# Performance work log

Measured on AMD Instinct MI355X. Metric: run time of the kernel, lower is better.

## Reference

```python
import math
import jax, jax.numpy as jnp
import numpy as np

N_HEAD = 16


def setup_inputs() -> dict:
    key = jax.random.key(0)
    ks = jax.random.split(key, 6)
    B, T, C = 4, 2048, 1024
    hs = C // N_HEAD
    block_size = 2048
    x = jax.random.normal(ks[0], (B, T, C), dtype=jnp.float32)
    c_attn_w = jax.random.normal(ks[1], (C, 3 * C), dtype=jnp.float32) * 0.02
    c_attn_b = jnp.zeros((3 * C,), dtype=jnp.float32)
    c_proj_w = jax.random.normal(ks[2], (C, C), dtype=jnp.float32) * (0.02 * (2 * 24) ** -0.5)
    c_proj_b = jnp.zeros((C,), dtype=jnp.float32)
    wpe = jax.random.normal(ks[3], (block_size, hs), dtype=jnp.float32) * 0.02
    return {"x": x, "c_attn_w": c_attn_w, "c_attn_b": c_attn_b,
            "c_proj_w": c_proj_w, "c_proj_b": c_proj_b, "wpe": wpe}


def reference(x, c_attn_w, c_attn_b, c_proj_w, c_proj_b, wpe):
    B, T, C = x.shape
    hs = C // N_HEAD
    # fused QKV projection
    qkv = x @ c_attn_w + c_attn_b            # [B, T, 3C]
    q, k, v = jnp.split(qkv, 3, axis=-1)
    pos_emb = wpe[:T]                        # [T, hs]
    # NOTE: faithful to original — raw reshape (not transpose) before the add
    q = (q.reshape(B, N_HEAD, T, hs) + pos_emb).reshape(B, T, N_HEAD, hs)
    k = (k.reshape(B, N_HEAD, T, hs) + pos_emb).reshape(B, T, N_HEAD, hs)
    v = v.reshape(B, T, N_HEAD, hs)
    # vanilla causal attention
    qt = jnp.transpose(q, (0, 2, 1, 3))      # [B, H, T, hs]
    kt = jnp.transpose(k, (0, 2, 3, 1))      # [B, H, hs, T]
    vt = jnp.transpose(v, (0, 2, 1, 3))      # [B, H, T, hs]
    att = qt @ kt / math.sqrt(hs)            # [B, H, T, T]
    causal = jnp.tril(jnp.ones((T, T), dtype=bool))
    att = jnp.where(causal, att, float('-inf'))
    att = jax.nn.softmax(att, axis=-1)
    y = att @ vt                             # [B, H, T, hs]
    y = jnp.transpose(y, (0, 2, 1, 3)).reshape(B, T, C)
    return y @ c_proj_w + c_proj_b
```

## Files before the change

kernel.cpp:

```cpp
#include <hip/hip_runtime.h>

typedef __attribute__((ext_vector_type(8))) short s16x8;
typedef __attribute__((ext_vector_type(4))) float f32x4;
typedef __attribute__((ext_vector_type(4))) unsigned short u16x4;

#define AS1 __attribute__((address_space(1)))
#define AS3 __attribute__((address_space(3)))

__device__ __forceinline__ unsigned short f2bf(float f) {
    union { float f; unsigned u; } c; c.f = f;
    return (unsigned short)((c.u + 0x7FFFu + ((c.u >> 16) & 1u)) >> 16);
}

__global__ void k_f32_to_bf16(const float* __restrict__ src,
                              unsigned short* __restrict__ dst, int n8) {
    int idx = blockIdx.x * 256 + threadIdx.x;
    int stride = gridDim.x * 256;
    for (int i = idx; i < n8; i += stride) {
        const float4* s = (const float4*)src + (size_t)i * 2;
        float4 a = s[0], b = s[1];
        s16x8 o;
        o[0] = (short)f2bf(a.x); o[1] = (short)f2bf(a.y);
        o[2] = (short)f2bf(a.z); o[3] = (short)f2bf(a.w);
        o[4] = (short)f2bf(b.x); o[5] = (short)f2bf(b.y);
        o[6] = (short)f2bf(b.z); o[7] = (short)f2bf(b.w);
        *((s16x8*)dst + i) = o;
    }
}

__global__ __launch_bounds__(256) void k_transpose_bf16(
    const float* __restrict__ W, unsigned short* __restrict__ Wt, int K, int N) {
    __shared__ float t[64][65];
    const int nk = K >> 6;
    const int k0 = (blockIdx.x % nk) << 6;
    const int n0 = (blockIdx.x / nk) << 6;
    const int tid = threadIdx.x;
#pragma unroll
    for (int it = 0; it < 4; it++) {
        int idx = tid + (it << 8);
        int r = idx >> 4, c4 = (idx & 15) << 2;
        float4 v = *(const float4*)(W + (size_t)(k0 + r) * N + n0 + c4);
        t[r][c4] = v.x; t[r][c4 + 1] = v.y; t[r][c4 + 2] = v.z; t[r][c4 + 3] = v.w;
    }
    __syncthreads();
#pragma unroll
    for (int it = 0; it < 2; it++) {
        int idx = tid + (it << 8);
        int rn = idx >> 3, c8 = (idx & 7) << 3;
        s16x8 o;
#pragma unroll
        for (int j = 0; j < 8; j++) o[j] = (short)f2bf(t[c8 + j][rn]);
        *(s16x8*)(Wt + (size_t)(n0 + rn) * K + k0 + c8) = o;
    }
}

__global__ __launch_bounds__(512, 2) void k_gemm_ring(
    const unsigned short* __restrict__ A, const unsigned short* __restrict__ Bt,
    const float* __restrict__ bias, const float* __restrict__ wpe,
    unsigned short* __restrict__ Qo, unsigned short* __restrict__ Ko,
    unsigned short* __restrict__ Vo, float* __restrict__ Fo,
    int N, int K, int mode) {
    __shared__ __align__(16) char smem[147456];
    const int tid = threadIdx.x;
    const int lane = tid & 63, wid = tid >> 6;
    const int wm = wid >> 2, wn = wid & 3;
    const int l15 = lane & 15, lg = lane >> 4;
    const int ntile = N >> 7;
    const int chunk = (int)gridDim.x >> 3;
    const int l = ((int)blockIdx.x & 7) * chunk + ((int)blockIdx.x >> 3);
    const int m0 = (l / ntile) << 8;
    const int n0 = (l % ntile) << 7;

    const int trow = tid >> 3, tcol = tid & 7;
    const unsigned short* pA[4];
    const unsigned short* pB[2];
#pragma unroll
    for (int i = 0; i < 4; i++) {
        int r = (i << 6) + trow;
        pA[i] = A + (size_t)(m0 + r) * K + ((tcol ^ (r & 7)) << 3);
    }
#pragma unroll
    for (int i = 0; i < 2; i++) {
        int r = (i << 6) + trow;
        pB[i] = Bt + (size_t)(n0 + r) * K + ((tcol ^ (r & 7)) << 3);
    }
    const int dA = tid << 4;

    int aoff[8][2], boff[2][2];
#pragma unroll
    for (int mi = 0; mi < 8; mi++) {
        int r = (wm << 7) + (mi << 4) + l15;
#pragma unroll
        for (int kk = 0; kk < 2; kk++)
            aoff[mi][kk] = r * 128 + (((lg + (kk << 2)) ^ (r & 7)) << 4);
    }
#pragma unroll
    for (int ni = 0; ni < 2; ni++) {
        int r = (wn << 5) + (ni << 4) + l15;
#pragma unroll
        for (int kk = 0; kk < 2; kk++)
            boff[ni][kk] = r * 128 + (((lg + (kk << 2)) ^ (r & 7)) << 4);
    }

    const f32x4 vzero = {0.f, 0.f, 0.f, 0.f};
    f32x4 acc[8][2];
#pragma unroll
    for (int i = 0; i < 8; i++) {
        acc[i][0] = vzero; acc[i][1] = vzero;
    }

    auto stage = [&](int slot) {
        char* ab = smem + slot * 32768;
        char* bb = smem + 98304 + slot * 16384;
#pragma unroll
        for (int i = 0; i < 4; i++) {
            __builtin_amdgcn_global_load_lds((const AS1 void*)pA[i],
                                             (AS3 void*)(ab + (i << 13) + dA),
                                             16, 0, 0);
            pA[i] += 64;
        }
#pragma unroll
        for (int i = 0; i < 2; i++) {
            __builtin_amdgcn_global_load_lds((const AS1 void*)pB[i],
                                             (AS3 void*)(bb + (i << 13) + dA),
                                             16, 0, 0);
            pB[i] += 64;
        }
    };

    const int NT = K >> 6;
    stage(0);
    stage(1);

    for (int c = 0; c < NT; c++) {
        if (c < NT - 1)
            asm volatile("s_waitcnt vmcnt(6)\ns_barrier" ::: "memory");
        else
            asm volatile("s_waitcnt vmcnt(0)\ns_barrier" ::: "memory");
        const int cs = c % 3;
        const char* ab = smem + cs * 32768;
        const char* bb = smem + 98304 + cs * 16384;

        s16x8 af[8], bfr[2];
#pragma unroll
        for (int mi = 0; mi < 8; mi++)
            af[mi] = *(const s16x8*)(ab + aoff[mi][0]);
#pragma unroll
        for (int ni = 0; ni < 2; ni++)
            bfr[ni] = *(const s16x8*)(bb + boff[ni][0]);
        if (c + 2 < NT) stage((c + 2) % 3);
        __builtin_amdgcn_s_setprio(1);
#pragma unroll
        for (int mi = 0; mi < 8; mi++)
#pragma unroll
            for (int ni = 0; ni < 2; ni++)
                acc[mi][ni] = __builtin_amdgcn_mfma_f32_16x16x32_bf16(
                    af[mi], bfr[ni], acc[mi][ni], 0, 0, 0);
        __builtin_amdgcn_s_setprio(0);
#pragma unroll
        for (int mi = 0; mi < 8; mi++)
            af[mi] = *(const s16x8*)(ab + aoff[mi][1]);
#pragma unroll
        for (int ni = 0; ni < 2; ni++)
            bfr[ni] = *(const s16x8*)(bb + boff[ni][1]);
        __builtin_amdgcn_s_setprio(1);
#pragma unroll
        for (int mi = 0; mi < 8; mi++)
#pragma unroll
            for (int ni = 0; ni < 2; ni++)
                acc[mi][ni] = __builtin_amdgcn_mfma_f32_16x16x32_bf16(
                    af[mi], bfr[ni], acc[mi][ni], 0, 0, 0);
        __builtin_amdgcn_s_setprio(0);
    }

    if (mode == 0) {
#pragma unroll
        for (int ni = 0; ni < 2; ni++) {
            int n = n0 + (wn << 5) + (ni << 4) + l15;
            int which = n >> 10, rem = n & 1023;
            int h = rem >> 6, s = rem & 63;
            unsigned short* outp = (which == 0) ? Qo : ((which == 1) ? Ko : Vo);
            float bv = bias[n];
#pragma unroll
            for (int mi = 0; mi < 8; mi++) {
#pragma unroll
                for (int j = 0; j < 4; j++) {
                    int m = m0 + (wm << 7) + (mi << 4) + (lg << 2) + j;
                    int b = m >> 11, t = m & 2047;
                    float v = acc[mi][ni][j] + bv;
                    if (which < 2) v += wpe[((((t << 4) + h) & 2047) << 6) + s];
                    outp[(size_t)(b * 16 + h) * 131072 + (size_t)t * 64 + s] = f2bf(v);
                }
            }
        }
    } else {
#pragma unroll
        for (int ni = 0; ni < 2; ni++) {
            int n = n0 + (wn << 5) + (ni << 4) + l15;
            float bv = bias[n];
#pragma unroll
            for (int mi = 0; mi < 8; mi++) {
#pragma unroll
                for (int j = 0; j < 4; j++) {
                    int m = m0 + (wm << 7) + (mi << 4) + (lg << 2) + j;
                    Fo[(size_t)m * N + n] = acc[mi][ni][j] + bv;
                }
            }
        }
    }
}

__global__ __launch_bounds__(256, 6) void k_attn(
    const unsigned short* __restrict__ Qg, const unsigned short* __restrict__ Kg,
    const unsigned short* __restrict__ Vg, unsigned short* __restrict__ Yg) {
    __shared__ unsigned short Klds[4096];
    __shared__ unsigned short Vtlds[4096];
    __shared__ unsigned short Plds[4096];
    const int tid = threadIdx.x, lane = tid & 63, wid = tid >> 6;
    const int l15 = lane & 15, lg = lane >> 4;
    const int lr = lane >> 3, ls = lane & 7;
    const int p = blockIdx.x;
    const int xcd = p & 7, rank = p >> 3;
    const int qt = 31 - (rank >> 3);
    const int bh = ((rank & 7) << 3) | xcd;
    const int b = bh >> 4, h = bh & 15;
    const size_t base = (size_t)bh * 131072;
    const int q0 = qt << 6;
    const int qrow = q0 + (wid << 4) + l15;
    const int vkv4 = (tid >> 4) << 2;
    const int vd4 = (tid & 15) << 2;

    const f32x4 vzero = {0.f, 0.f, 0.f, 0.f};

    s16x8 qf[2];
#pragma unroll
    for (int kk = 0; kk < 2; kk++)
        qf[kk] = *(const s16x8*)(Qg + base + (size_t)qrow * 64 +
                                 (kk << 5) + (lg << 3));

    f32x4 o[4];
#pragma unroll
    for (int i = 0; i < 4; i++) o[i] = vzero;
    float mrun = -3.0e38f, lrun = 0.f;

    const int nt = qt + 1;
    for (int tI = 0; tI < nt; tI++) {
        const int kv0 = tI << 6;
#pragma unroll
        for (int i = 0; i < 2; i++) {
            int r = (wid << 4) + (i << 3) + lr;
            int sl = (ls ^ (r & 7)) << 3;
            __builtin_amdgcn_global_load_lds(
                (const AS1 void*)(Kg + base + (size_t)(kv0 + r) * 64 + sl),
                (AS3 void*)(Klds + (wid << 10) + (i << 9)), 16, 0, 0);
        }
        {
            u16x4 vv[4];
#pragma unroll
            for (int r = 0; r < 4; r++)
                vv[r] = *(const u16x4*)(Vg + base +
                                        (size_t)(kv0 + vkv4 + r) * 64 + vd4);
#pragma unroll
            for (int dj = 0; dj < 4; dj++) {
                int row = vd4 + dj;
                int fv = (row ^ (row >> 3)) & 7;
                unsigned long long pk =
                    (unsigned long long)vv[0][dj] |
                    ((unsigned long long)vv[1][dj] << 16) |
                    ((unsigned long long)vv[2][dj] << 32) |
                    ((unsigned long long)vv[3][dj] << 48);
                *(unsigned long long*)((char*)Vtlds + row * 128 +
                                       ((((vkv4 >> 3) ^ fv) & 7) << 4) +
                                       ((vkv4 & 7) << 1)) = pk;
            }
        }
        __syncthreads();

        f32x4 sacc[4];
#pragma unroll
        for (int i = 0; i < 4; i++) sacc[i] = vzero;
        __builtin_amdgcn_s_setprio(1);
#pragma unroll
        for (int kk = 0; kk < 2; kk++) {
            s16x8 kf[4];
#pragma unroll
            for (int ki = 0; ki < 4; ki++) {
                int row = (ki << 4) + l15;
                int slot = lg + (kk << 2);
                kf[ki] = *(const s16x8*)((const char*)Klds + row * 128 +
                                         ((slot ^ (row & 7)) << 4));
            }
#pragma unroll
            for (int ki = 0; ki < 4; ki++)
                sacc[ki] = __builtin_amdgcn_mfma_f32_16x16x32_bf16(
                    kf[ki], qf[kk], sacc[ki], 0, 0, 0);
        }
        __builtin_amdgcn_s_setprio(0);

        float tm = -3.0e38f;
        if (tI == nt - 1) {
#pragma unroll
            for (int ki = 0; ki < 4; ki++) {
#pragma unroll
                for (int j = 0; j < 4; j++) {
                    int kvg = kv0 + (ki << 4) + (lg << 2) + j;
                    float sv = sacc[ki][j];
                    if (kvg > qrow) sv = -3.0e38f;
                    sacc[ki][j] = sv;
                    tm = fmaxf(tm, sv);
                }
            }
        } else {
#pragma unroll
            for (int ki = 0; ki < 4; ki++) {
#pragma unroll
                for (int j = 0; j < 4; j++) tm = fmaxf(tm, sacc[ki][j]);
            }
        }
        tm = fmaxf(tm, __shfl_xor(tm, 16, 64));
        tm = fmaxf(tm, __shfl_xor(tm, 32, 64));
        float mnew = fmaxf(mrun, tm);
        float rfac = __expf((mrun - mnew) * 0.125f);
        float m8 = mnew * 0.125f;
        mrun = mnew;
        float ps = 0.f;
#pragma unroll
        for (int ki = 0; ki < 4; ki++) {
#pragma unroll
            for (int j = 0; j < 4; j++) {
                float pv = __expf(__builtin_fmaf(sacc[ki][j], 0.125f, -m8));
                sacc[ki][j] = pv;
                ps += pv;
            }
        }
        ps += __shfl_xor(ps, 16, 64);
        ps += __shfl_xor(ps, 32, 64);
        lrun = lrun * rfac + ps;
#pragma unroll
        for (int j = 0; j < 4; j++) {
            float rj = __shfl(rfac, (lane & 48) | ((lg << 2) + j), 64);
#pragma unroll
            for (int si = 0; si < 4; si++) o[si][j] *= rj;
        }
#pragma unroll
        for (int ki = 0; ki < 4; ki++) {
            unsigned long long pk =
                (unsigned long long)f2bf(sacc[ki][0]) |
                ((unsigned long long)f2bf(sacc[ki][1]) << 16) |
                ((unsigned long long)f2bf(sacc[ki][2]) << 32) |
                ((unsigned long long)f2bf(sacc[ki][3]) << 48);
            int kvl = (ki << 4) + (lg << 2);
            int slot = kvl >> 3;
            *(unsigned long long*)((char*)Plds + (wid << 11) + l15 * 128 +
                                   ((slot ^ (l15 & 7)) << 4) +
                                   ((kvl & 7) << 1)) = pk;
        }

        __builtin_amdgcn_s_setprio(1);
#pragma unroll
        for (int kk = 0; kk < 2; kk++) {
            s16x8 vf[4];
#pragma unroll
            for (int si = 0; si < 4; si++) {
                int row = (si << 4) + l15;
                int slot = lg + (kk << 2);
                int fv = (row ^ (row >> 3)) & 7;
                vf[si] = *(const s16x8*)((const char*)Vtlds + row * 128 +
                                         (((slot ^ fv) & 7) << 4));
            }
            int prow = l15;
            int slot = lg + (kk << 2);
            s16x8 pf = *(const s16x8*)((const char*)Plds + (wid << 11) +
                                       prow * 128 + ((slot ^ (prow & 7)) << 4));
#pragma unroll
            for (int si = 0; si < 4; si++)
                o[si] = __builtin_amdgcn_mfma_f32_16x16x32_bf16(
                    pf, vf[si], o[si], 0, 0, 0);
        }
        __builtin_amdgcn_s_setprio(0);
        __syncthreads();
    }

#pragma unroll
    for (int j = 0; j < 4; j++) {
        float lv = __shfl(lrun, (lane & 48) | ((lg << 2) + j), 64);
        float linv = 1.0f / lv;
        int qg = q0 + (wid << 4) + (lg << 2) + j;
        size_t rowoff = ((size_t)b * 2048 + qg) * 1024 + (h << 6);
#pragma unroll
        for (int si = 0; si < 4; si++) {
            int sg = (si << 4) + l15;
            Yg[rowoff + sg] = f2bf(o[si][j] * linv);
        }
    }
}

extern "C" void kernel_launch(void* const* d_in, const int* in_sizes, int n_in,
                              void* d_out, int out_size, void* d_ws, size_t ws_size,
                              hipStream_t stream) {
    const float* x   = (const float*)d_in[0];
    const float* w1  = (const float*)d_in[1];
    const float* b1  = (const float*)d_in[2];
    const float* w2  = (const float*)d_in[3];
    const float* b2  = (const float*)d_in[4];
    const float* wpe = (const float*)d_in[5];
    float* out = (float*)d_out;

    char* ws = (char*)d_ws;
    unsigned short* xb  = (unsigned short*)(ws);
    unsigned short* w1t = (unsigned short*)(ws + 16777216);
    unsigned short* w2t = (unsigned short*)(ws + 23068672);
    unsigned short* Qb  = (unsigned short*)(ws + 25165824);
    unsigned short* Kb  = (unsigned short*)(ws + 41943040);
    unsigned short* Vb  = (unsigned short*)(ws + 58720256);
    unsigned short* Yb  = (unsigned short*)(ws + 75497472);

    k_f32_to_bf16<<<2048, 256, 0, stream>>>(x, xb, 8388608 / 8);
    k_transpose_bf16<<<768, 256, 0, stream>>>(w1, w1t, 1024, 3072);
    k_transpose_bf16<<<256, 256, 0, stream>>>(w2, w2t, 1024, 1024);
    k_gemm_ring<<<768, 512, 0, stream>>>(xb, w1t, b1, wpe, Qb, Kb, Vb,
                                         nullptr, 3072, 1024, 0);
    k_attn<<<2048, 256, 0, stream>>>(Qb, Kb, Vb, Yb);
    k_gemm_ring<<<256, 512, 0, stream>>>(Yb, w2t, b2, nullptr, nullptr, nullptr,
                                         nullptr, out, 1024, 1024, 1);
}
```

Before: 304.6 us.

## Reshape GEMM warp tiling to 4x2 grid with split-phase prefetch

The GEMM warp grid changes from 2x4 to 4x2, so each wave computes a 64x64 subtile (4x4 MFMA fragments) instead of 128x32. This cuts the LDS fragment reads per MFMA. The next-stage global-to-LDS prefetch is split into two halves issued around an extra mid-iteration barrier, which interleaves the loads with the two MFMA phases. The cost is an additional barrier per K step, and all A fragments now stay held in registers for the whole iteration.

```diff
diff --git a/kernel.cpp b/kernel.cpp
--- a/kernel.cpp
+++ b/kernel.cpp
@@ -63,7 +63,7 @@
     __shared__ __align__(16) char smem[147456];
     const int tid = threadIdx.x;
     const int lane = tid & 63, wid = tid >> 6;
-    const int wm = wid >> 2, wn = wid & 3;
+    const int wm = wid >> 1, wn = wid & 1;
     const int l15 = lane & 15, lg = lane >> 4;
     const int ntile = N >> 7;
     const int chunk = (int)gridDim.x >> 3;
@@ -86,106 +86,128 @@
     }
     const int dA = tid << 4;
 
-    int aoff[8][2], boff[2][2];
-#pragma unroll
-    for (int mi = 0; mi < 8; mi++) {
-        int r = (wm << 7) + (mi << 4) + l15;
+    int aoff[4][2], boff[4][2];
+#pragma unroll
+    for (int mi = 0; mi < 4; mi++) {
+        int r = (wm << 6) + (mi << 4) + l15;
 #pragma unroll
         for (int kk = 0; kk < 2; kk++)
             aoff[mi][kk] = r * 128 + (((lg + (kk << 2)) ^ (r & 7)) << 4);
     }
 #pragma unroll
-    for (int ni = 0; ni < 2; ni++) {
-        int r = (wn << 5) + (ni << 4) + l15;
+    for (int ni = 0; ni < 4; ni++) {
+        int r = (wn << 6) + (ni << 4) + l15;
 #pragma unroll
         for (int kk = 0; kk < 2; kk++)
             boff[ni][kk] = r * 128 + (((lg + (kk << 2)) ^ (r & 7)) << 4);
     }
 
     const f32x4 vzero = {0.f, 0.f, 0.f, 0.f};
-    f32x4 acc[8][2];
-#pragma unroll
-    for (int i = 0; i < 8; i++) {
-        acc[i][0] = vzero; acc[i][1] = vzero;
-    }
-
-    auto stage = [&](int slot) {
+    f32x4 acc[4][4];
+#pragma unroll
+    for (int i = 0; i < 4; i++)
+#pragma unroll
+        for (int j = 0; j < 4; j++) acc[i][j] = vzero;
+
+    auto stageH0 = [&](int slot) {
         char* ab = smem + slot * 32768;
         char* bb = smem + 98304 + slot * 16384;
-#pragma unroll
-        for (int i = 0; i < 4; i++) {
-            __builtin_amdgcn_global_load_lds((const AS1 void*)pA[i],
-                                             (AS3 void*)(ab + (i << 13) + dA),
-                                             16, 0, 0);
-            pA[i] += 64;
-        }
-#pragma unroll
-        for (int i = 0; i < 2; i++) {
-            __builtin_amdgcn_global_load_lds((const AS1 void*)pB[i],
-                                             (AS3 void*)(bb + (i << 13) + dA),
-                                             16, 0, 0);
-            pB[i] += 64;
-        }
+        __builtin_amdgcn_global_load_lds((const AS1 void*)pA[0],
+                                         (AS3 void*)(ab + dA), 16, 0, 0);
+        pA[0] += 64;
+        __builtin_amdgcn_global_load_lds((const AS1 void*)pA[1],
+                                         (AS3 void*)(ab + 8192 + dA), 16, 0, 0);
+        pA[1] += 64;
+        __builtin_amdgcn_global_load_lds((const AS1 void*)pB[0],
+                                         (AS3 void*)(bb + dA), 16, 0, 0);
+        pB[0] += 64;
     };
+    auto stageH1 = [&](int slot) {
+        char* ab = smem + slot * 32768;
+        char* bb = smem + 98304 + slot * 16384;
+        __builtin_amdgcn_global_load_lds((const AS1 void*)pA[2],
+                                         (AS3 void*)(ab + 16384 + dA), 16, 0, 0);
+        pA[2] += 64;
+        __builtin_amdgcn_global_load_lds((const AS1 void*)pA[3],
+                                         (AS3 void*)(ab + 24576 + dA), 16, 0, 0);
+        pA[3] += 64;
+        __builtin_amdgcn_global_load_lds((const AS1 void*)pB[1],
+                                         (AS3 void*)(bb + 8192 + dA), 16, 0, 0);
+        pB[1] += 64;
+    };
 
     const int NT = K >> 6;
-    stage(0);
-    stage(1);
+    stageH0(0); stageH1(0);
+    stageH0(1); stageH1(1);
 
     for (int c = 0; c < NT; c++) {
         if (c < NT - 1)
-            asm volatile("s_waitcnt vmcnt(6)\ns_barrier" ::: "memory");
+            asm volatile("s_waitcnt vmcnt(6)" ::: "memory");
         else
-            asm volatile("s_waitcnt vmcnt(0)\ns_barrier" ::: "memory");
+            asm volatile("s_waitcnt vmcnt(0)" ::: "memory");
+        __builtin_amdgcn_s_barrier();
         const int cs = c % 3;
         const char* ab = smem + cs * 32768;
         const char* bb = smem + 98304 + cs * 16384;
-
-        s16x8 af[8], bfr[2];
-#pragma unroll
-        for (int mi = 0; mi < 8; mi++)
-            af[mi] = *(const s16x8*)(ab + aoff[mi][0]);
+        const bool pf = (c + 2 < NT);
+        const int ps = (c + 2) % 3;
+
+        s16x8 af[4][2], bf0[2][2];
+#pragma unroll
+        for (int mi = 0; mi < 4; mi++)
+#pragma unroll
+            for (int kk = 0; kk < 2; kk++)
+                af[mi][kk] = *(const s16x8*)(ab + aoff[mi][kk]);
 #pragma unroll
         for (int ni = 0; ni < 2; ni++)
-            bfr[ni] = *(const s16x8*)(bb + boff[ni][0]);
-        if (c + 2 < NT) stage((c + 2) % 3);
+#pragma unroll
+            for (int kk = 0; kk < 2; kk++)
+                bf0[ni][kk] = *(const s16x8*)(bb + boff[ni][kk]);
+        if (pf) stageH0(ps);
         __builtin_amdgcn_s_setprio(1);
 #pragma unroll
-        for (int mi = 0; mi < 8; mi++)
-#pragma unroll
-            for (int ni = 0; ni < 2; ni++)
-                acc[mi][ni] = __builtin_amdgcn_mfma_f32_16x16x32_bf16(
-                    af[mi], bfr[ni], acc[mi][ni], 0, 0, 0);
+        for (int kk = 0; kk < 2; kk++)
+#pragma unroll
+            for (int mi = 0; mi < 4; mi++)
+#pragma unroll
+                for (int ni = 0; ni < 2; ni++)
+                    acc[mi][ni] = __builtin_amdgcn_mfma_f32_16x16x32_bf16(
+                        af[mi][kk], bf0[ni][kk], acc[mi][ni], 0, 0, 0);
         __builtin_amdgcn_s_setprio(0);
-#pragma unroll
-        for (int mi = 0; mi < 8; mi++)
-            af[mi] = *(const s16x8*)(ab + aoff[mi][1]);
+        __builtin_amdgcn_s_barrier();
+
+        s16x8 bf1[2][2];
 #pragma unroll
         for (int ni = 0; ni < 2; ni++)
-            bfr[ni] = *(const s16x8*)(bb + boff[ni][1]);
+#pragma unroll
+            for (int kk = 0; kk < 2; kk++)
+                bf1[ni][kk] = *(const s16x8*)(bb + boff[2 + ni][kk]);
+        if (pf) stageH1(ps);
         __builtin_amdgcn_s_setprio(1);
 #pragma unroll
-        for (int mi = 0; mi < 8; mi++)
-#pragma unroll
-            for (int ni = 0; ni < 2; ni++)
-                acc[mi][ni] = __builtin_amdgcn_mfma_f32_16x16x32_bf16(
-                    af[mi], bfr[ni], acc[mi][ni], 0, 0, 0);
+        for (int kk = 0; kk < 2; kk++)
+#pragma unroll
+            for (int mi = 0; mi < 4; mi++)
+#pragma unroll
+                for (int ni = 0; ni < 2; ni++)
+                    acc[mi][2 + ni] = __builtin_amdgcn_mfma_f32_16x16x32_bf16(
+                        af[mi][kk], bf1[ni][kk], acc[mi][2 + ni], 0, 0, 0);
         __builtin_amdgcn_s_setprio(0);
     }
 
     if (mode == 0) {
 #pragma unroll
-        for (int ni = 0; ni < 2; ni++) {
-            int n = n0 + (wn << 5) + (ni << 4) + l15;
+        for (int ni = 0; ni < 4; ni++) {
+            int n = n0 + (wn << 6) + (ni << 4) + l15;
             int which = n >> 10, rem = n & 1023;
             int h = rem >> 6, s = rem & 63;
             unsigned short* outp = (which == 0) ? Qo : ((which == 1) ? Ko : Vo);
             float bv = bias[n];
 #pragma unroll
-            for (int mi = 0; mi < 8; mi++) {
+            for (int mi = 0; mi < 4; mi++) {
 #pragma unroll
                 for (int j = 0; j < 4; j++) {
-                    int m = m0 + (wm << 7) + (mi << 4) + (lg << 2) + j;
+                    int m = m0 + (wm << 6) + (mi << 4) + (lg << 2) + j;
                     int b = m >> 11, t = m & 2047;
                     float v = acc[mi][ni][j] + bv;
                     if (which < 2) v += wpe[((((t << 4) + h) & 2047) << 6) + s];
@@ -195,14 +217,14 @@
         }
     } else {
 #pragma unroll
-        for (int ni = 0; ni < 2; ni++) {
-            int n = n0 + (wn << 5) + (ni << 4) + l15;
+        for (int ni = 0; ni < 4; ni++) {
+            int n = n0 + (wn << 6) + (ni << 4) + l15;
             float bv = bias[n];
 #pragma unroll
-            for (int mi = 0; mi < 8; mi++) {
+            for (int mi = 0; mi < 4; mi++) {
 #pragma unroll
                 for (int j = 0; j < 4; j++) {
-                    int m = m0 + (wm << 7) + (mi << 4) + (lg << 2) + j;
+                    int m = m0 + (wm << 6) + (mi << 4) + (lg << 2) + j;
                     Fo[(size_t)m * N + n] = acc[mi][ni][j] + bv;
                 }
             }
```

After: 301.0 us. About the same (-1.2%).
